# Kernel optimization log

Measured on AMD Instinct MI355X. Metric: run time of the kernel, lower is better.

## Reference

```python
import jax, jax.numpy as jnp
import numpy as np

N, E, F, H, G, C = 50000, 800000, 128, 64, 512, 10
RATIO = 0.5  # forward arg `ratio` baked as constant


def seg_mean(msgs, idx, n):
    s = jax.ops.segment_sum(msgs, idx, num_segments=n)
    cnt = jax.ops.segment_sum(jnp.ones(idx.shape[0], msgs.dtype), idx, num_segments=n)
    return s / jnp.maximum(cnt, 1.0)[:, None]


def sage(x, src, dst, Wl, bl, Wr, ew=None):
    # PyG SAGEConv: lin_l(mean_{j->i} msg_j) + lin_r(x_i); weighted variant scales messages
    m = x[src] if ew is None else x[src] * ew[:, None]
    agg = seg_mean(m, dst, x.shape[0])
    return agg @ Wl + bl + x @ Wr


def topk_mask(scores, seg, num_graphs, ratio):
    # per-graph (segment) top-k edge selection: keep ceil(ratio*edges_in_graph) highest scores
    e = scores.shape[0]
    counts = jax.ops.segment_sum(jnp.ones(e, jnp.float32), seg, num_segments=num_graphs)
    order = jnp.lexsort((-scores, seg))  # sort by segment, then score descending
    seg_sorted = seg[order]
    starts = jnp.concatenate([jnp.zeros(1, jnp.float32), jnp.cumsum(counts)[:-1]])
    rank = jnp.arange(e, dtype=jnp.float32) - starts[seg_sorted]
    k = jnp.ceil(ratio * counts)
    sel = (rank < k[seg_sorted]).astype(scores.dtype)
    return jnp.zeros(e, scores.dtype).at[order].set(sel)


def setup_inputs():
    key = jax.random.key(0)
    ks = jax.random.split(key, 16)
    w = lambda k, shape, fan: (jax.random.normal(k, shape, jnp.float32) / np.sqrt(fan))
    return {
        'x': jax.random.normal(ks[0], (N, F), jnp.float32),
        'edge_index': jax.random.randint(ks[1], (2, E), 0, N, jnp.int32),
        'batch': jnp.sort(jax.random.randint(ks[2], (N,), 0, G, jnp.int32)),
        'W1l': w(ks[3], (F, H), F), 'b1l': jnp.zeros(H, jnp.float32), 'W1r': w(ks[4], (F, H), F),
        'W2l': w(ks[5], (H, H), H), 'b2l': jnp.zeros(H, jnp.float32), 'W2r': w(ks[6], (H, H), H),
        'W3l': w(ks[7], (H, H), H), 'b3l': jnp.zeros(H, jnp.float32), 'W3r': w(ks[8], (H, H), H),
        'Wlin1': w(ks[9], (H, H), H), 'blin1': jnp.zeros(H, jnp.float32),
        'Wlin2': w(ks[10], (H, C), H), 'blin2': jnp.zeros(C, jnp.float32),
    }


def reference(x, edge_index, batch, W1l, b1l, W1r, W2l, b2l, W2r, W3l, b3l, W3r, Wlin1, blin1, Wlin2, blin2):
    src, dst = edge_index[0], edge_index[1]
    h = jax.nn.relu(sage(x, src, dst, W1l, b1l, W1r))
    edge_scores = jnp.sum(h[src] * h[dst], axis=-1)  # [E]
    seg = batch[src]  # graph id per edge (sections)
    sampled = topk_mask(edge_scores, seg, G, RATIO)
    ew = edge_scores * sampled
    h = jax.nn.relu(sage(h, src, dst, W2l, b2l, W2r, ew))
    h = jax.nn.relu(sage(h, src, dst, W3l, b3l, W3r, ew))
    pooled = seg_mean(h, batch, G)  # global_mean_pool
    z = jax.nn.relu(pooled @ Wlin1 + blin1)
    z = z @ Wlin2 + blin2  # dropout inactive in eval
    return jax.nn.log_softmax(z, axis=-1), sampled
```

## Files before the change

### kernel.cpp

```cpp
#include <hip/hip_runtime.h>
#include <hip/hip_bf16.h>
#include <math.h>

static constexpr int N = 50000;
static constexpr int E = 800000;
static constexpr int F = 128;
static constexpr int H = 64;
static constexpr int G = 512;
static constexpr int C = 10;
static constexpr int CAP = 256;

static inline int cdiv(long a, int b) { return (int)((a + b - 1) / b); }

__device__ __forceinline__ float uinv_score(unsigned u) {
  return (u & 0x80000000u) ? __uint_as_float(u & 0x7fffffffu) : __uint_as_float(~u);
}

__global__ void k_deg_goff(const int* __restrict__ dst, const int* __restrict__ batch,
                           int* __restrict__ deg, int* __restrict__ goff) {
  for (int i = blockIdx.x * 256 + threadIdx.x; i < N; i += gridDim.x * 256) {
    int b = batch[i];
    if (i == 0) {
      for (int g = 0; g <= b; ++g) goff[g] = 0;
    } else {
      int p = batch[i - 1];
      for (int g = p + 1; g <= b; ++g) goff[g] = i;
    }
    if (i == N - 1) {
      for (int g = b + 1; g <= G; ++g) goff[g] = N;
    }
  }
  for (int e = blockIdx.x * 256 + threadIdx.x; e < E; e += gridDim.x * 256)
    atomicAdd(&deg[dst[e]], 1);
}

__global__ void k_scan_a(const int* __restrict__ cnt, int* __restrict__ off,
                         int* __restrict__ bsum, int n) {
  __shared__ int wsum[16];
  int tid = threadIdx.x, lane = tid & 63, wv = tid >> 6;
  int idx = blockIdx.x * 4096 + tid * 4;
  int v0 = (idx + 0 < n) ? cnt[idx + 0] : 0;
  int v1 = (idx + 1 < n) ? cnt[idx + 1] : 0;
  int v2 = (idx + 2 < n) ? cnt[idx + 2] : 0;
  int v3 = (idx + 3 < n) ? cnt[idx + 3] : 0;
  int local = v0 + v1 + v2 + v3;
  int inc = local;
  for (int d = 1; d < 64; d <<= 1) {
    int t = __shfl_up(inc, d);
    if (lane >= d) inc += t;
  }
  if (lane == 63) wsum[wv] = inc;
  __syncthreads();
  if (tid < 16) {
    int t = wsum[tid];
    for (int d = 1; d < 16; d <<= 1) {
      int u = __shfl_up(t, d);
      if (tid >= d) t += u;
    }
    wsum[tid] = t;
  }
  __syncthreads();
  int woff = (wv > 0) ? wsum[wv - 1] : 0;
  int excl = woff + inc - local;
  if (idx + 0 < n) off[idx + 0] = excl;
  if (idx + 1 < n) off[idx + 1] = excl + v0;
  if (idx + 2 < n) off[idx + 2] = excl + v0 + v1;
  if (idx + 3 < n) off[idx + 3] = excl + v0 + v1 + v2;
  if (tid == 0) bsum[blockIdx.x] = wsum[15];
}

__global__ void k_scan_b(int* __restrict__ bsum, int nb) {
  int lane = threadIdx.x;
  int v = (lane < nb) ? bsum[lane] : 0;
  int inc = v;
  for (int d = 1; d < 64; d <<= 1) {
    int t = __shfl_up(inc, d);
    if (lane >= d) inc += t;
  }
  if (lane < nb) bsum[lane] = inc - v;
  if (lane == nb) bsum[nb] = inc;
}

__global__ void k_scan_c(int* __restrict__ off, int* __restrict__ cursor,
                         const int* __restrict__ bsum, int n, int nb) {
  int i = blockIdx.x * 256 + threadIdx.x;
  if (i < n) {
    int v = off[i] + bsum[i >> 12];
    off[i] = v;
    cursor[i] = v;
  } else if (i == n) {
    off[n] = bsum[nb];
  }
}

__global__ void k_fill_csr(const int* __restrict__ src, const int* __restrict__ dst,
                           int* __restrict__ cursor, int2* __restrict__ csr,
                           int* __restrict__ einv, int lo, int hi) {
  int e = blockIdx.x * 256 + threadIdx.x;
  if (e >= E) return;
  int d = dst[e];
  if (d < lo || d >= hi) return;
  int slot = atomicAdd(&cursor[d], 1);
  csr[slot] = make_int2(src[e], e);
  einv[e] = slot;
}

template <int K>
__global__ void k_gemm2(const float* __restrict__ in, const float* __restrict__ Wl,
                        const float* __restrict__ Wr, const float* __restrict__ b,
                        float* __restrict__ y, float* __restrict__ r) {
  __shared__ float sx[16][K];
  int lane = threadIdx.x, ty = threadIdx.y;
  int tid = ty * 64 + lane;
  int row0 = blockIdx.x * 16;
  const float4* gsrc = (const float4*)(in + (size_t)row0 * K);
  float4* sdst = (float4*)(&sx[0][0]);
#pragma unroll
  for (int i = tid; i < 16 * K / 4; i += 256) sdst[i] = gsrc[i];
  __syncthreads();
  float al[4], ar[4];
  float bias = b[lane];
#pragma unroll
  for (int j = 0; j < 4; ++j) { al[j] = 0.f; ar[j] = bias; }
#pragma unroll 4
  for (int f = 0; f < K; ++f) {
    float wl = Wl[f * H + lane];
    float wr = Wr[f * H + lane];
#pragma unroll
    for (int j = 0; j < 4; ++j) {
      float xv = sx[ty * 4 + j][f];
      al[j] += xv * wl;
      ar[j] += xv * wr;
    }
  }
#pragma unroll
  for (int j = 0; j < 4; ++j) {
    int row = row0 + ty * 4 + j;
    y[(size_t)row * H + lane] = al[j];
    r[(size_t)row * H + lane] = ar[j];
  }
}

template <int K>
__global__ void k_gemm2h(const float* __restrict__ in, const float* __restrict__ Wl,
                         const float* __restrict__ Wr, const float* __restrict__ b,
                         __hip_bfloat16* __restrict__ y, float* __restrict__ r) {
  __shared__ float sx[16][K];
  int lane = threadIdx.x, ty = threadIdx.y;
  int tid = ty * 64 + lane;
  int row0 = blockIdx.x * 16;
  const float4* gsrc = (const float4*)(in + (size_t)row0 * K);
  float4* sdst = (float4*)(&sx[0][0]);
#pragma unroll
  for (int i = tid; i < 16 * K / 4; i += 256) sdst[i] = gsrc[i];
  __syncthreads();
  float al[4], ar[4];
  float bias = b[lane];
#pragma unroll
  for (int j = 0; j < 4; ++j) { al[j] = 0.f; ar[j] = bias; }
#pragma unroll 4
  for (int f = 0; f < K; ++f) {
    float wl = Wl[f * H + lane];
    float wr = Wr[f * H + lane];
#pragma unroll
    for (int j = 0; j < 4; ++j) {
      float xv = sx[ty * 4 + j][f];
      al[j] += xv * wl;
      ar[j] += xv * wr;
    }
  }
#pragma unroll
  for (int j = 0; j < 4; ++j) {
    int row = row0 + ty * 4 + j;
    y[(size_t)row * H + lane] = __float2bfloat16(al[j]);
    r[(size_t)row * H + lane] = ar[j];
  }
}

__global__ void k_agg1(const float* __restrict__ y, const float* __restrict__ r,
                       const int2* __restrict__ csr, const int* __restrict__ off,
                       float* __restrict__ out) {
  int node = blockIdx.x * 8 + threadIdx.y;
  int lane = threadIdx.x;
  int q = lane >> 3, c = lane & 7;
  int s0 = off[node], s1 = off[node + 1];
  float4 a0 = make_float4(0.f, 0.f, 0.f, 0.f);
  float4 a1 = make_float4(0.f, 0.f, 0.f, 0.f);
  int i = s0 + q;
  for (; i + 8 < s1; i += 16) {
    int2 se0 = csr[i];
    int2 se1 = csr[i + 8];
    const float4* p0 = (const float4*)(y + (size_t)se0.x * H);
    const float4* p1 = (const float4*)(y + (size_t)se1.x * H);
    float4 u0 = p0[c], v0 = p0[c + 8];
    float4 u1 = p1[c], v1 = p1[c + 8];
    a0.x += u0.x + u1.x; a0.y += u0.y + u1.y; a0.z += u0.z + u1.z; a0.w += u0.w + u1.w;
    a1.x += v0.x + v1.x; a1.y += v0.y + v1.y; a1.z += v0.z + v1.z; a1.w += v0.w + v1.w;
  }
  for (; i < s1; i += 8) {
    int2 se = csr[i];
    const float4* p = (const float4*)(y + (size_t)se.x * H);
    float4 u = p[c], v = p[c + 8];
    a0.x += u.x; a0.y += u.y; a0.z += u.z; a0.w += u.w;
    a1.x += v.x; a1.y += v.y; a1.z += v.z; a1.w += v.w;
  }
#pragma unroll
  for (int d = 8; d < 64; d <<= 1) {
    a0.x += __shfl_xor(a0.x, d); a0.y += __shfl_xor(a0.y, d);
    a0.z += __shfl_xor(a0.z, d); a0.w += __shfl_xor(a0.w, d);
    a1.x += __shfl_xor(a1.x, d); a1.y += __shfl_xor(a1.y, d);
    a1.z += __shfl_xor(a1.z, d); a1.w += __shfl_xor(a1.w, d);
  }
  if (q == 0) {
    float inv = 1.f / fmaxf((float)(s1 - s0), 1.f);
    const float4* rp = (const float4*)(r + (size_t)node * H);
    float4 r0 = rp[c], r1 = rp[c + 8];
    float4 o0, o1;
    o0.x = fmaxf(a0.x * inv + r0.x, 0.f); o0.y = fmaxf(a0.y * inv + r0.y, 0.f);
    o0.z = fmaxf(a0.z * inv + r0.z, 0.f); o0.w = fmaxf(a0.w * inv + r0.w, 0.f);
    o1.x = fmaxf(a1.x * inv + r1.x, 0.f); o1.y = fmaxf(a1.y * inv + r1.y, 0.f);
    o1.z = fmaxf(a1.z * inv + r1.z, 0.f); o1.w = fmaxf(a1.w * inv + r1.w, 0.f);
    float4* op = (float4*)(out + (size_t)node * H);
    op[c] = o0; op[c + 8] = o1;
  }
}

__global__ void k_agg_w(const __hip_bfloat16* __restrict__ y, const float* __restrict__ r,
                        const int2* __restrict__ csr, const float* __restrict__ ewc,
                        const int* __restrict__ off, float* __restrict__ out) {
  int node = blockIdx.x * 8 + threadIdx.y;
  int lane = threadIdx.x;
  int q = lane >> 3, c = lane & 7;
  int s0 = off[node], s1 = off[node + 1];
  float a[8] = {0.f, 0.f, 0.f, 0.f, 0.f, 0.f, 0.f, 0.f};
  int i = s0 + q;
  for (; i + 8 < s1; i += 16) {
    int2 se0 = csr[i];
    int2 se1 = csr[i + 8];
    float w0 = ewc[i];
    float w1 = ewc[i + 8];
    if (w0 != 0.f) {
      uint4 pk = ((const uint4*)((const unsigned short*)y + (size_t)se0.x * H))[c];
      a[0] += w0 * __uint_as_float(pk.x << 16); a[1] += w0 * __uint_as_float(pk.x & 0xffff0000u);
      a[2] += w0 * __uint_as_float(pk.y << 16); a[3] += w0 * __uint_as_float(pk.y & 0xffff0000u);
      a[4] += w0 * __uint_as_float(pk.z << 16); a[5] += w0 * __uint_as_float(pk.z & 0xffff0000u);
      a[6] += w0 * __uint_as_float(pk.w << 16); a[7] += w0 * __uint_as_float(pk.w & 0xffff0000u);
    }
    if (w1 != 0.f) {
      uint4 pk = ((const uint4*)((const unsigned short*)y + (size_t)se1.x * H))[c];
      a[0] += w1 * __uint_as_float(pk.x << 16); a[1] += w1 * __uint_as_float(pk.x & 0xffff0000u);
      a[2] += w1 * __uint_as_float(pk.y << 16); a[3] += w1 * __uint_as_float(pk.y & 0xffff0000u);
      a[4] += w1 * __uint_as_float(pk.z << 16); a[5] += w1 * __uint_as_float(pk.z & 0xffff0000u);
      a[6] += w1 * __uint_as_float(pk.w << 16); a[7] += w1 * __uint_as_float(pk.w & 0xffff0000u);
    }
  }
  for (; i < s1; i += 8) {
    int2 se = csr[i];
    float w = ewc[i];
    if (w != 0.f) {
      uint4 pk = ((const uint4*)((const unsigned short*)y + (size_t)se.x * H))[c];
      a[0] += w * __uint_as_float(pk.x << 16); a[1] += w * __uint_as_float(pk.x & 0xffff0000u);
      a[2] += w * __uint_as_float(pk.y << 16); a[3] += w * __uint_as_float(pk.y & 0xffff0000u);
      a[4] += w * __uint_as_float(pk.z << 16); a[5] += w * __uint_as_float(pk.z & 0xffff0000u);
      a[6] += w * __uint_as_float(pk.w << 16); a[7] += w * __uint_as_float(pk.w & 0xffff0000u);
    }
  }
#pragma unroll
  for (int d = 8; d < 64; d <<= 1) {
#pragma unroll
    for (int j = 0; j < 8; ++j) a[j] += __shfl_xor(a[j], d);
  }
  if (q == 0) {
    float inv = 1.f / fmaxf((float)(s1 - s0), 1.f);
    const float4* rp = (const float4*)(r + (size_t)node * H);
    float4 r0 = rp[2 * c], r1 = rp[2 * c + 1];
    float4 o0, o1;
    o0.x = fmaxf(a[0] * inv + r0.x, 0.f); o0.y = fmaxf(a[1] * inv + r0.y, 0.f);
    o0.z = fmaxf(a[2] * inv + r0.z, 0.f); o0.w = fmaxf(a[3] * inv + r0.w, 0.f);
    o1.x = fmaxf(a[4] * inv + r1.x, 0.f); o1.y = fmaxf(a[5] * inv + r1.y, 0.f);
    o1.z = fmaxf(a[6] * inv + r1.z, 0.f); o1.w = fmaxf(a[7] * inv + r1.w, 0.f);
    float4* op = (float4*)(out + (size_t)node * H);
    op[2 * c] = o0; op[2 * c + 1] = o1;
  }
}

__global__ void k_score_csr(const float* __restrict__ h1, const int2* __restrict__ csr,
                            const int* __restrict__ off, const int* __restrict__ batch,
                            unsigned* __restrict__ scoreu_csr,
                            unsigned short* __restrict__ seg_csr, int* __restrict__ hist) {
  int node = blockIdx.x * 8 + threadIdx.y;
  int lane = threadIdx.x;
  int q = lane >> 4, c = lane & 15;
  int s0 = off[node], s1 = off[node + 1];
  float4 hn = ((const float4*)(h1 + (size_t)node * H))[c];
  int i = s0 + q;
  for (; i + 4 < s1; i += 8) {
    int2 se0 = csr[i];
    int2 se1 = csr[i + 4];
    float4 hs0 = ((const float4*)(h1 + (size_t)se0.x * H))[c];
    float4 hs1 = ((const float4*)(h1 + (size_t)se1.x * H))[c];
    float p0 = hn.x * hs0.x + hn.y * hs0.y + hn.z * hs0.z + hn.w * hs0.w;
    float p1 = hn.x * hs1.x + hn.y * hs1.y + hn.z * hs1.z + hn.w * hs1.w;
    p0 += __shfl_xor(p0, 1); p1 += __shfl_xor(p1, 1);
    p0 += __shfl_xor(p0, 2); p1 += __shfl_xor(p1, 2);
    p0 += __shfl_xor(p0, 4); p1 += __shfl_xor(p1, 4);
    p0 += __shfl_xor(p0, 8); p1 += __shfl_xor(p1, 8);
    if (c == 0) {
      int g0 = batch[se0.x], g1 = batch[se1.x];
      unsigned u0 = __float_as_uint(p0); u0 = (u0 & 0x80000000u) ? ~u0 : (u0 | 0x80000000u);
      unsigned u1 = __float_as_uint(p1); u1 = (u1 & 0x80000000u) ? ~u1 : (u1 | 0x80000000u);
      scoreu_csr[i] = u0; scoreu_csr[i + 4] = u1;
      seg_csr[i] = (unsigned short)g0; seg_csr[i + 4] = (unsigned short)g1;
      atomicAdd(&hist[g0 * 256 + (int)(u0 >> 24)], 1);
      atomicAdd(&hist[g1 * 256 + (int)(u1 >> 24)], 1);
    }
  }
  for (; i < s1; i += 4) {
    int2 se = csr[i];
    float4 hs = ((const float4*)(h1 + (size_t)se.x * H))[c];
    float p = hn.x * hs.x + hn.y * hs.y + hn.z * hs.z + hn.w * hs.w;
    p += __shfl_xor(p, 1);
    p += __shfl_xor(p, 2);
    p += __shfl_xor(p, 4);
    p += __shfl_xor(p, 8);
    if (c == 0) {
      int g = batch[se.x];
      unsigned u = __float_as_uint(p);
      u = (u & 0x80000000u) ? ~u : (u | 0x80000000u);
      scoreu_csr[i] = u;
      seg_csr[i] = (unsigned short)g;
      atomicAdd(&hist[g * 256 + (int)(u >> 24)], 1);
    }
  }
}

__global__ void k_hist(const unsigned* __restrict__ scoreu, const unsigned short* __restrict__ seg,
                       const unsigned* __restrict__ prefix, int* __restrict__ hist, int pass) {
  int e = blockIdx.x * 256 + threadIdx.x;
  if (e >= E) return;
  unsigned u = scoreu[e];
  int g = (int)seg[e];
  int predshift = 32 - 8 * pass;
  if ((u >> predshift) == (prefix[g] >> predshift))
    atomicAdd(&hist[g * 256 + (int)((u >> (24 - 8 * pass)) & 0xFFu)], 1);
}

__global__ void k_scan(int* __restrict__ hist, unsigned* __restrict__ prefix,
                       int* __restrict__ krem, int pass) {
  int g = blockIdx.x;
  int lane = threadIdx.x;
  int4* row = (int4*)(hist + (size_t)g * 256);
  int4 v = row[lane];
  int vj[4] = {v.x, v.y, v.z, v.w};
  int s = v.x + v.y + v.z + v.w;
  int inc = s;
  for (int d = 1; d < 64; d <<= 1) {
    int t = __shfl_up(inc, d);
    if (lane >= d) inc += t;
  }
  int T = __shfl(inc, 63);
  int k = (pass == 0) ? ((T + 1) >> 1) : krem[g];
  int excl = inc - s;
  int pre[4] = {excl, excl + vj[0], excl + vj[0] + vj[1], excl + vj[0] + vj[1] + vj[2]};
  int bsel_l = -1, newk_l = 0;
  if (k > 0) {
    for (int j = 3; j >= 0; --j) {
      int suf = T - pre[j];
      if (suf >= k) { bsel_l = 4 * lane + j; newk_l = k - (suf - vj[j]); break; }
    }
  }
  unsigned long long mask = __ballot(bsel_l >= 0);
  int bsel = 255, newk = 0;
  if (k > 0 && mask) {
    int hi = 63 - __builtin_clzll(mask);
    bsel = __shfl(bsel_l, hi);
    newk = __shfl(newk_l, hi);
  }
  if (lane == 0) {
    unsigned base = (pass == 0) ? 0u : prefix[g];
    prefix[g] = base | ((unsigned)bsel << (24 - 8 * pass));
    krem[g] = newk;
  }
  row[lane] = make_int4(0, 0, 0, 0);
}

__global__ void k_select(const unsigned* __restrict__ scoreu_csr,
                         const unsigned short* __restrict__ seg_csr,
                         const unsigned* __restrict__ thresh,
                         int* __restrict__ eqcnt, int* __restrict__ eqlist,
                         unsigned char* __restrict__ sel_csr, float* __restrict__ ew_csr) {
  int s = blockIdx.x * 256 + threadIdx.x;
  if (s >= E) return;
  unsigned u = scoreu_csr[s];
  int g = (int)seg_csr[s];
  unsigned t = thresh[g];
  unsigned um = u & 0xffffff00u;
  float sel = 0.f;
  if (um > t) sel = 1.f;
  else if (um == t) {
    int slot = atomicAdd(&eqcnt[g], 1);
    if (slot < CAP) eqlist[g * CAP + slot] = s;
  }
  sel_csr[s] = (unsigned char)sel;
  ew_csr[s] = uinv_score(u) * sel;
}

__global__ void k_resolve(const int* __restrict__ krem, const int* __restrict__ eqcnt,
                          const int* __restrict__ eqlist, const int2* __restrict__ csr,
                          const unsigned* __restrict__ scoreu_csr,
                          unsigned char* __restrict__ sel_csr, float* __restrict__ ew_csr) {
  int g = blockIdx.x * 256 + threadIdx.x;
  if (g >= G) return;
  int c = eqcnt[g]; if (c > CAP) c = CAP;
  int r = krem[g];  if (r > c) r = c;
  const int* lst = eqlist + g * CAP;
  unsigned last_u = 0u; int last_e = -1; bool first = true;
  for (int i = 0; i < r; ++i) {
    unsigned bu = 0u; int be = -1, bs = -1;
    for (int j = 0; j < c; ++j) {
      int slot = lst[j];
      unsigned u = scoreu_csr[slot];
      int eid = csr[slot].y;
      bool after = first || (u < last_u) || (u == last_u && eid > last_e);
      if (after && (bs < 0 || u > bu || (u == bu && eid < be))) { bu = u; be = eid; bs = slot; }
    }
    if (bs < 0) break;
    sel_csr[bs] = 1;
    ew_csr[bs] = uinv_score(bu);
    last_u = bu; last_e = be; first = false;
  }
}

__global__ void k_sampled(const int* __restrict__ einv, const unsigned char* __restrict__ sel_csr,
                          float* __restrict__ sampled) {
  int e = (blockIdx.x * 256 + threadIdx.x) * 4;
  if (e >= E) return;
  int4 iv = *(const int4*)(einv + e);
  float4 o;
  o.x = (float)sel_csr[iv.x];
  o.y = (float)sel_csr[iv.y];
  o.z = (float)sel_csr[iv.z];
  o.w = (float)sel_csr[iv.w];
  *(float4*)(sampled + e) = o;
}

__global__ void k_poolhead(const float* __restrict__ h3, const int* __restrict__ goff,
                           const float* __restrict__ W1, const float* __restrict__ b1,
                           const float* __restrict__ W2, const float* __restrict__ b2,
                           float* __restrict__ outp) {
  int g = blockIdx.x;
  int h = threadIdx.x;
  int s0 = goff[g], s1 = goff[g + 1];
  float a = 0.f;
  for (int n = s0; n < s1; ++n) a += h3[(size_t)n * H + h];
  float inv = 1.f / fmaxf((float)(s1 - s0), 1.f);
  __shared__ float p[H], z1[H], z2[C];
  __shared__ float lse;
  p[h] = a * inv;
  __syncthreads();
  float acc = b1[h];
#pragma unroll 8
  for (int f = 0; f < H; ++f) acc += p[f] * W1[f * H + h];
  z1[h] = fmaxf(acc, 0.f);
  __syncthreads();
  if (h < C) {
    float a2 = b2[h];
#pragma unroll 8
    for (int f = 0; f < H; ++f) a2 += z1[f] * W2[f * C + h];
    z2[h] = a2;
  }
  __syncthreads();
  if (h == 0) {
    float m = z2[0];
    for (int c = 1; c < C; ++c) m = fmaxf(m, z2[c]);
    float s = 0.f;
    for (int c = 0; c < C; ++c) s += expf(z2[c] - m);
    lse = m + logf(s);
  }
  __syncthreads();
  if (h < C) outp[(size_t)g * C + h] = z2[h] - lse;
}

extern "C" void kernel_launch(void* const* d_in, const int* in_sizes, int n_in,
                              void* d_out, int out_size, void* d_ws, size_t ws_size,
                              hipStream_t stream) {
  const float* x     = (const float*)d_in[0];
  const int*   ei    = (const int*)d_in[1];
  const int*   batch = (const int*)d_in[2];
  const float* W1l   = (const float*)d_in[3];
  const float* b1l   = (const float*)d_in[4];
  const float* W1r   = (const float*)d_in[5];
  const float* W2l   = (const float*)d_in[6];
  const float* b2l   = (const float*)d_in[7];
  const float* W2r   = (const float*)d_in[8];
  const float* W3l   = (const float*)d_in[9];
  const float* b3l   = (const float*)d_in[10];
  const float* W3r   = (const float*)d_in[11];
  const float* Wlin1 = (const float*)d_in[12];
  const float* blin1 = (const float*)d_in[13];
  const float* Wlin2 = (const float*)d_in[14];
  const float* blin2 = (const float*)d_in[15];

  const int* srcv = ei;
  const int* dstv = ei + E;

  float* out_ls   = (float*)d_out;
  float* out_samp = out_ls + G * C;

  char* w = (char*)d_ws;
  auto carve = [&](size_t bytes) { void* p = (void*)w; w += (bytes + 255) & ~(size_t)255; return p; };
  char* zbase   = w;
  int*      deg     = (int*)carve((size_t)N * 4);
  int*      eqcnt   = (int*)carve((size_t)G * 4);
  int*      hist    = (int*)carve((size_t)G * 256 * 4);
  size_t    zbytes  = (size_t)(w - zbase);
  float*    h1      = (float*)carve((size_t)N * H * 4);
  float*    h2      = (float*)carve((size_t)N * H * 4);
  float*    h3      = (float*)carve((size_t)N * H * 4);
  float*    yb      = (float*)carve((size_t)N * H * 4);
  float*    rb      = (float*)carve((size_t)N * H * 4);
  __hip_bfloat16* ybh = (__hip_bfloat16*)carve((size_t)N * H * 2);
  unsigned* scoreu_csr = (unsigned*)carve((size_t)E * 4);
  unsigned short* seg_csr = (unsigned short*)carve((size_t)E * 2);
  float*    ew_csr     = (float*)carve((size_t)E * 4);
  unsigned char* sel_csr = (unsigned char*)carve((size_t)E);
  int2*     csr     = (int2*)carve((size_t)E * 8);
  int*      einv    = (int*)carve((size_t)E * 4);
  int*      off     = (int*)carve((size_t)(N + 1) * 4);
  int*      cursor  = (int*)carve((size_t)N * 4);
  int*      goff    = (int*)carve((size_t)(G + 1) * 4);
  unsigned* prefix  = (unsigned*)carve((size_t)G * 4);
  int*      krem    = (int*)carve((size_t)G * 4);
  int*      eqlist  = (int*)carve((size_t)G * CAP * 4);
  int*      bsum    = (int*)carve((size_t)16 * 4);

  hipMemsetAsync(zbase, 0, zbytes, stream);

  k_deg_goff<<<128, 256, 0, stream>>>(dstv, batch, deg, goff);
  int nb = cdiv(N, 4096);
  k_scan_a<<<nb, 1024, 0, stream>>>(deg, off, bsum, N);
  k_scan_b<<<1, 64, 0, stream>>>(bsum, nb);
  k_scan_c<<<cdiv(N + 1, 256), 256, 0, stream>>>(off, cursor, bsum, N, nb);
  k_fill_csr<<<cdiv(E, 256), 256, 0, stream>>>(srcv, dstv, cursor, csr, einv, 0, N / 2);
  k_fill_csr<<<cdiv(E, 256), 256, 0, stream>>>(srcv, dstv, cursor, csr, einv, N / 2, N);

  k_gemm2<F><<<N / 16, dim3(64, 4), 0, stream>>>(x, W1l, W1r, b1l, yb, rb);
  k_agg1<<<N / 8, dim3(64, 8), 0, stream>>>(yb, rb, csr, off, h1);

  k_score_csr<<<N / 8, dim3(64, 8), 0, stream>>>(h1, csr, off, batch,
                                                 scoreu_csr, seg_csr, hist);
  k_scan<<<G, 64, 0, stream>>>(hist, prefix, krem, 0);
  for (int p = 1; p <= 2; ++p) {
    k_hist<<<cdiv(E, 256), 256, 0, stream>>>(scoreu_csr, seg_csr, prefix, hist, p);
    k_scan<<<G, 64, 0, stream>>>(hist, prefix, krem, p);
  }
  k_select<<<cdiv(E, 256), 256, 0, stream>>>(scoreu_csr, seg_csr, prefix,
                                             eqcnt, eqlist, sel_csr, ew_csr);
  k_resolve<<<cdiv(G, 256), 256, 0, stream>>>(krem, eqcnt, eqlist, csr, scoreu_csr,
                                              sel_csr, ew_csr);
  k_sampled<<<cdiv(E / 4, 256), 256, 0, stream>>>(einv, sel_csr, out_samp);

  k_gemm2h<H><<<N / 16, dim3(64, 4), 0, stream>>>(h1, W2l, W2r, b2l, ybh, rb);
  k_agg_w<<<N / 8, dim3(64, 8), 0, stream>>>(ybh, rb, csr, ew_csr, off, h2);

  k_gemm2h<H><<<N / 16, dim3(64, 4), 0, stream>>>(h2, W3l, W3r, b3l, ybh, rb);
  k_agg_w<<<N / 8, dim3(64, 8), 0, stream>>>(ybh, rb, csr, ew_csr, off, h3);

  k_poolhead<<<G, 64, 0, stream>>>(h3, goff, Wlin1, blin1, Wlin2, blin2, out_ls);
}
```

Measured before the change: 497.9 us.

## Compact selected edges into per-node list before weighted aggregations

Adds a compaction kernel that builds, for each destination node, a packed list of only the selected edges, storing source index and edge weight together in one int2, with per-node offsets taken from an atomic cursor. The two weighted aggregation kernels then walk this half-size list instead of scanning all edges and branching on zero weights. This cuts the CSR and weight reads and the divergent branches in both layer-2 and layer-3 aggregations. The cost is one extra kernel pass over the edges, plus atomic-ordered offsets that may place nodes' lists non-contiguously; the list reuses the yb buffer as storage.

```diff
diff --git a/kernel.cpp b/kernel.cpp
--- a/kernel.cpp
+++ b/kernel.cpp
@@ -225,45 +225,57 @@
   }
 }
 
+__global__ void k_compact(const unsigned char* __restrict__ sel,
+                          const int2* __restrict__ csr, const float* __restrict__ ewc,
+                          const int* __restrict__ off, int* __restrict__ cursor2,
+                          int2* __restrict__ csr2, int* __restrict__ off2,
+                          int* __restrict__ cnt2) {
+  int node = blockIdx.x * 8 + threadIdx.y;
+  int lane = threadIdx.x;
+  int s0 = off[node], s1 = off[node + 1];
+  unsigned long long lt = ((unsigned long long)1 << lane) - 1;
+  int c = 0;
+  for (int i = s0 + lane; i < s1; i += 64) c += sel[i] ? 1 : 0;
+#pragma unroll
+  for (int d = 1; d < 64; d <<= 1) c += __shfl_xor(c, d);
+  int base = 0;
+  if (lane == 0) {
+    base = atomicAdd(cursor2, c);
+    off2[node] = base;
+    cnt2[node] = c;
+  }
+  base = __shfl(base, 0);
+  int cum = 0;
+  for (int i0 = s0; i0 < s1; i0 += 64) {
+    int i = i0 + lane;
+    bool f = (i < s1) && sel[i];
+    unsigned long long m = __ballot(f);
+    if (f) {
+      int rank = __popcll(m & lt);
+      int2 se = csr[i];
+      csr2[base + cum + rank] = make_int2(se.x, __float_as_int(ewc[i]));
+    }
+    cum += __popcll(m);
+  }
+}
+
 __global__ void k_agg_w(const __hip_bfloat16* __restrict__ y, const float* __restrict__ r,
-                        const int2* __restrict__ csr, const float* __restrict__ ewc,
-                        const int* __restrict__ off, float* __restrict__ out) {
+                        const int2* __restrict__ csr2, const int* __restrict__ off2,
+                        const int* __restrict__ cnt2, const int* __restrict__ off,
+                        float* __restrict__ out) {
   int node = blockIdx.x * 8 + threadIdx.y;
   int lane = threadIdx.x;
   int q = lane >> 3, c = lane & 7;
-  int s0 = off[node], s1 = off[node + 1];
+  int b0 = off2[node], cn = cnt2[node];
   float a[8] = {0.f, 0.f, 0.f, 0.f, 0.f, 0.f, 0.f, 0.f};
-  int i = s0 + q;
-  for (; i + 8 < s1; i += 16) {
-    int2 se0 = csr[i];
-    int2 se1 = csr[i + 8];
-    float w0 = ewc[i];
-    float w1 = ewc[i + 8];
-    if (w0 != 0.f) {
-      uint4 pk = ((const uint4*)((const unsigned short*)y + (size_t)se0.x * H))[c];
-      a[0] += w0 * __uint_as_float(pk.x << 16); a[1] += w0 * __uint_as_float(pk.x & 0xffff0000u);
-      a[2] += w0 * __uint_as_float(pk.y << 16); a[3] += w0 * __uint_as_float(pk.y & 0xffff0000u);
-      a[4] += w0 * __uint_as_float(pk.z << 16); a[5] += w0 * __uint_as_float(pk.z & 0xffff0000u);
-      a[6] += w0 * __uint_as_float(pk.w << 16); a[7] += w0 * __uint_as_float(pk.w & 0xffff0000u);
-    }
-    if (w1 != 0.f) {
-      uint4 pk = ((const uint4*)((const unsigned short*)y + (size_t)se1.x * H))[c];
-      a[0] += w1 * __uint_as_float(pk.x << 16); a[1] += w1 * __uint_as_float(pk.x & 0xffff0000u);
-      a[2] += w1 * __uint_as_float(pk.y << 16); a[3] += w1 * __uint_as_float(pk.y & 0xffff0000u);
-      a[4] += w1 * __uint_as_float(pk.z << 16); a[5] += w1 * __uint_as_float(pk.z & 0xffff0000u);
-      a[6] += w1 * __uint_as_float(pk.w << 16); a[7] += w1 * __uint_as_float(pk.w & 0xffff0000u);
-    }
-  }
-  for (; i < s1; i += 8) {
-    int2 se = csr[i];
-    float w = ewc[i];
-    if (w != 0.f) {
-      uint4 pk = ((const uint4*)((const unsigned short*)y + (size_t)se.x * H))[c];
-      a[0] += w * __uint_as_float(pk.x << 16); a[1] += w * __uint_as_float(pk.x & 0xffff0000u);
-      a[2] += w * __uint_as_float(pk.y << 16); a[3] += w * __uint_as_float(pk.y & 0xffff0000u);
-      a[4] += w * __uint_as_float(pk.z << 16); a[5] += w * __uint_as_float(pk.z & 0xffff0000u);
-      a[6] += w * __uint_as_float(pk.w << 16); a[7] += w * __uint_as_float(pk.w & 0xffff0000u);
-    }
+  for (int j = q; j < cn; j += 8) {
+    int2 sw = csr2[b0 + j];
+    float w = __int_as_float(sw.y);
+    uint4 pk = ((const uint4*)((const unsigned short*)y + (size_t)sw.x * H))[c];
+    a[0] += w * __uint_as_float(pk.x << 16); a[1] += w * __uint_as_float(pk.x & 0xffff0000u);
+    a[2] += w * __uint_as_float(pk.y << 16); a[3] += w * __uint_as_float(pk.y & 0xffff0000u);
+    a[4] += w * __uint_as_float(pk.z << 16); a[5] += w * __uint_as_float(pk.z & 0xffff0000u);
+    a[6] += w * __uint_as_float(pk.w << 16); a[7] += w * __uint_as_float(pk.w & 0xffff0000u);
   }
 #pragma unroll
   for (int d = 8; d < 64; d <<= 1) {
@@ -271,7 +283,8 @@
     for (int j = 0; j < 8; ++j) a[j] += __shfl_xor(a[j], d);
   }
   if (q == 0) {
-    float inv = 1.f / fmaxf((float)(s1 - s0), 1.f);
+    int degn = off[node + 1] - off[node];
+    float inv = 1.f / fmaxf((float)degn, 1.f);
     const float4* rp = (const float4*)(r + (size_t)node * H);
     float4 r0 = rp[2 * c], r1 = rp[2 * c + 1];
     float4 o0, o1;
@@ -512,6 +525,7 @@
   char* zbase   = w;
   int*      deg     = (int*)carve((size_t)N * 4);
   int*      eqcnt   = (int*)carve((size_t)G * 4);
+  int*      cursor2 = (int*)carve(256);
   int*      hist    = (int*)carve((size_t)G * 256 * 4);
   size_t    zbytes  = (size_t)(w - zbase);
   float*    h1      = (float*)carve((size_t)N * H * 4);
@@ -528,11 +542,14 @@
   int*      einv    = (int*)carve((size_t)E * 4);
   int*      off     = (int*)carve((size_t)(N + 1) * 4);
   int*      cursor  = (int*)carve((size_t)N * 4);
+  int*      off2    = (int*)carve((size_t)N * 4);
+  int*      cnt2    = (int*)carve((size_t)N * 4);
   int*      goff    = (int*)carve((size_t)(G + 1) * 4);
   unsigned* prefix  = (unsigned*)carve((size_t)G * 4);
   int*      krem    = (int*)carve((size_t)G * 4);
   int*      eqlist  = (int*)carve((size_t)G * CAP * 4);
   int*      bsum    = (int*)carve((size_t)16 * 4);
+  int2*     csr2    = (int2*)yb;
 
   hipMemsetAsync(zbase, 0, zbytes, stream);
 
@@ -560,11 +577,14 @@
                                               sel_csr, ew_csr);
   k_sampled<<<cdiv(E / 4, 256), 256, 0, stream>>>(einv, sel_csr, out_samp);
 
+  k_compact<<<N / 8, dim3(64, 8), 0, stream>>>(sel_csr, csr, ew_csr, off, cursor2,
+                                               csr2, off2, cnt2);
+
   k_gemm2h<H><<<N / 16, dim3(64, 4), 0, stream>>>(h1, W2l, W2r, b2l, ybh, rb);
-  k_agg_w<<<N / 8, dim3(64, 8), 0, stream>>>(ybh, rb, csr, ew_csr, off, h2);
+  k_agg_w<<<N / 8, dim3(64, 8), 0, stream>>>(ybh, rb, csr2, off2, cnt2, off, h2);
 
   k_gemm2h<H><<<N / 16, dim3(64, 4), 0, stream>>>(h2, W3l, W3r, b3l, ybh, rb);
-  k_agg_w<<<N / 8, dim3(64, 8), 0, stream>>>(ybh, rb, csr, ew_csr, off, h3);
+  k_agg_w<<<N / 8, dim3(64, 8), 0, stream>>>(ybh, rb, csr2, off2, cnt2, off, h3);
 
   k_poolhead<<<G, 64, 0, stream>>>(h3, goff, Wlin1, blin1, Wlin2, blin2, out_ls);
 }
```

After: 1.063 ms. 113% more time.
